# Kernel tuning notes

Hardware: AMD Instinct MI355X
Metric: run time of the kernel (lower is better)

The kernel has to match this reference:

```python
import jax, jax.numpy as jnp
import numpy as np
import math

EMBED_DIM = 1024
NUM_HEADS = 16
D_K = EMBED_DIM // NUM_HEADS
B, S = 2, 2048


def setup_inputs() -> dict:
    key = jax.random.key(0)
    ks = jax.random.split(key, 6)
    scale = 1.0 / math.sqrt(EMBED_DIM)
    x = jax.random.normal(ks[0], (B, S, EMBED_DIM), dtype=jnp.float32)
    mask = jax.random.randint(ks[1], (B, S), 0, 2) > 0  # True = masked-out key
    wq = jax.random.normal(ks[2], (EMBED_DIM, EMBED_DIM), dtype=jnp.float32) * scale
    wk = jax.random.normal(ks[3], (EMBED_DIM, EMBED_DIM), dtype=jnp.float32) * scale
    wv = jax.random.normal(ks[4], (EMBED_DIM, EMBED_DIM), dtype=jnp.float32) * scale
    wo = jax.random.normal(ks[5], (EMBED_DIM, EMBED_DIM), dtype=jnp.float32) * scale
    return {"x": x, "mask": mask, "wq": wq, "wk": wk, "wv": wv, "wo": wo}


def reference(x, mask, wq, wk, wv, wo):
    b, s, _ = x.shape
    # torch nn.Linear(bias=False): y = x @ W.T
    q = (x @ wq.T).reshape(b, s, NUM_HEADS, D_K).transpose(0, 2, 1, 3)  # [B,H,S,Dk]
    k = (x @ wk.T).reshape(b, s, NUM_HEADS, D_K).transpose(0, 2, 1, 3)
    v = (x @ wv.T).reshape(b, s, NUM_HEADS, D_K).transpose(0, 2, 1, 3)
    scores = jnp.einsum('bhqd,bhkd->bhqk', q, k) / math.sqrt(D_K)
    # mask [B,S] -> [B,1,1,S]: key-padding mask, True filled with -1e9
    scores = jnp.where(mask[:, None, None, :], jnp.float32(-1e9), scores)
    attn = jax.nn.softmax(scores, axis=-1)
    # dropout in eval mode -> identity
    out = jnp.einsum('bhqk,bhkd->bhqd', attn, v)
    out = out.transpose(0, 2, 1, 3).reshape(b, s, EMBED_DIM)
    return out @ wo.T
```

## Files before the change

kernel.cpp:

```cpp
#include <hip/hip_runtime.h>
#include <hip/hip_bf16.h>


typedef unsigned short u16;
typedef unsigned int u32;
using short8 = __attribute__((ext_vector_type(8))) short;
using f32x4  = __attribute__((ext_vector_type(4))) float;

#define WS_XB    0u
#define WS_WQKV  8388608u
#define WS_WOB   14680064u
#define WS_QB    16777216u
#define WS_KB    25165824u
#define WS_VTB   33554432u
#define WS_OB    41943040u

__device__ __forceinline__ u16 f2bf(float f) {
  u32 u = __float_as_uint(f);
  u += 0x7fffu + ((u >> 16) & 1u);
  return (u16)(u >> 16);
}

__device__ __forceinline__ ushort4 pk4(f32x4 v) {
  ushort4 r; r.x = f2bf(v[0]); r.y = f2bf(v[1]); r.z = f2bf(v[2]); r.w = f2bf(v[3]);
  return r;
}

__device__ __forceinline__ u32 pkbf2(float lo, float hi) {
  union { __hip_bfloat162 b; u32 u; } c;
  c.b = __float22bfloat162_rn(make_float2(lo, hi));
  return c.u;
}

__device__ __forceinline__ void gload16(const void* g, void* l) {
  __builtin_amdgcn_global_load_lds(
      (const __attribute__((address_space(1))) u32*)g,
      (__attribute__((address_space(3))) u32*)l, 16, 0, 0);
}

#define KSCALE 0.18033688011112042f

__global__ void convert_k(const float* __restrict__ x, const float* __restrict__ wq,
                          const float* __restrict__ wk, const float* __restrict__ wv,
                          const float* __restrict__ wo,
                          u16* __restrict__ xb, u16* __restrict__ wqkv, u16* __restrict__ wob) {
  size_t g = ((size_t)blockIdx.x * 256 + threadIdx.x) * 4;
  const float* s; u16* d;
  if (g < 4194304u)      { s = x  + g;            d = xb   + g; }
  else if (g < 5242880u) { s = wq + (g - 4194304u); d = wqkv + (g - 4194304u); }
  else if (g < 6291456u) { s = wk + (g - 5242880u); d = wqkv + 1048576u + (g - 5242880u); }
  else if (g < 7340032u) { s = wv + (g - 6291456u); d = wqkv + 2097152u + (g - 6291456u); }
  else                   { s = wo + (g - 7340032u); d = wob  + (g - 7340032u); }
  float4 v = *(const float4*)s;
  f32x4 vv = {v.x, v.y, v.z, v.w};
  *(ushort4*)d = pk4(vv);
}

__global__ void gemm_qkv(const u16* __restrict__ A, const u16* __restrict__ Bt,
                         u16* __restrict__ qb, u16* __restrict__ kb, u16* __restrict__ vtb) {
  __shared__ __align__(16) u16 As[128 * 64];
  __shared__ __align__(16) u16 Bs[128 * 64];
  const int tid  = threadIdx.x;
  const int wave = tid >> 6, lane = tid & 63;
  const int c16  = lane & 15, quad = lane >> 4;
  const int tile_m = blockIdx.x * 128;
  const int tile_n = blockIdx.y * 128;
  const int wm = (wave >> 1) * 64, wn = (wave & 1) * 64;
  const int srow = wave * 32 + (lane >> 3);
  const int sc   = lane & 7;
  const int which = blockIdx.y >> 3;
  const bool swp  = (which < 2);

  const u16* Pa = swp ? Bs : As;
  const u16* Pb = swp ? As : Bs;
  const int  ra = swp ? wn : wm;
  const int  rb = swp ? wm : wn;

  f32x4 acc[4][4] = {};

  for (int k0 = 0; k0 < 1024; k0 += 64) {
    __syncthreads();
#pragma unroll
    for (int j = 0; j < 4; ++j) {
      int row = srow + j * 8;
      int cp  = sc ^ (row & 7);
      gload16(A  + (size_t)(tile_m + row) * 1024 + k0 + cp * 8, As + row * 64 + sc * 8);
      gload16(Bt + (size_t)(tile_n + row) * 1024 + k0 + cp * 8, Bs + row * 64 + sc * 8);
    }
    __syncthreads();
#pragma unroll
    for (int kc = 0; kc < 2; ++kc) {
      const int ch = ((kc * 4 + quad) ^ (c16 & 7)) * 8;
      short8 fa[4], fb[4];
#pragma unroll
      for (int i = 0; i < 4; ++i)
        fa[i] = *(const short8*)(Pa + (ra + i * 16 + c16) * 64 + ch);
#pragma unroll
      for (int j = 0; j < 4; ++j)
        fb[j] = *(const short8*)(Pb + (rb + j * 16 + c16) * 64 + ch);
#pragma unroll
      for (int i = 0; i < 4; ++i)
#pragma unroll
        for (int j = 0; j < 4; ++j)
          acc[i][j] = __builtin_amdgcn_mfma_f32_16x16x32_bf16(fa[i], fb[j], acc[i][j], 0, 0, 0);
    }
  }

  if (which == 2) {
#pragma unroll
    for (int i = 0; i < 4; ++i) {
      int m0 = tile_m + wm + i * 16 + quad * 4;
      int bb = m0 >> 11, ss0 = m0 & 2047;
#pragma unroll
      for (int j = 0; j < 4; ++j) {
        int f = (tile_n & 1023) + wn + j * 16 + c16;
        int h = f >> 6, d = f & 63;
        *(ushort4*)(vtb + ((size_t)(bb * 16 + h) * 64 + d) * 2048 + ss0) = pk4(acc[i][j]);
      }
    }
  } else {
    u16* dstb = which ? kb : qb;
#pragma unroll
    for (int i = 0; i < 4; ++i) {
      int full = (tile_n & 1023) + wn + i * 16 + quad * 4;
      int h = full >> 6, d0 = full & 63;
#pragma unroll
      for (int j = 0; j < 4; ++j) {
        int t = tile_m + wm + j * 16 + c16;
        int bb = t >> 11, ss = t & 2047;
        f32x4 v = acc[i][j];
        if (which == 0) { v[0] *= KSCALE; v[1] *= KSCALE; v[2] *= KSCALE; v[3] *= KSCALE; }
        *(ushort4*)(dstb + ((size_t)(bb * 16 + h) * 2048 + ss) * 64 + d0) = pk4(v);
      }
    }
  }
}

__global__ __launch_bounds__(256) void attn_k(const u16* __restrict__ qb, const u16* __restrict__ kb,
                                              const u16* __restrict__ vtb, const int* __restrict__ mask,
                                              u16* __restrict__ ob) {
  __shared__ __align__(16) u16 Ks[2][64 * 64];
  __shared__ __align__(16) u16 Vs[2][64 * 64];
  __shared__ __align__(16) u16 Ps[128 * 64];
  __shared__ u32 mask2[1024];

  const int tid  = threadIdx.x;
  const int wave = tid >> 6, lane = tid & 63;
  const int c16  = lane & 15, g4 = lane >> 4;
  const int bh   = blockIdx.y;
  const int bidx = bh >> 4, h = bh & 15;
  const int q0   = blockIdx.x * 128;

  {
    int4 m0 = *(const int4*)(mask + bidx * 2048 + tid * 8);
    int4 m1 = *(const int4*)(mask + bidx * 2048 + tid * 8 + 4);
    uint4 dd;
    dd.x = (m0.x ? 0u : 0xFFFFu) | (m0.y ? 0u : 0xFFFF0000u);
    dd.y = (m0.z ? 0u : 0xFFFFu) | (m0.w ? 0u : 0xFFFF0000u);
    dd.z = (m1.x ? 0u : 0xFFFFu) | (m1.y ? 0u : 0xFFFF0000u);
    dd.w = (m1.z ? 0u : 0xFFFFu) | (m1.w ? 0u : 0xFFFF0000u);
    *(uint4*)(mask2 + tid * 4) = dd;
  }

  const u16* qg = qb + ((size_t)bh * 2048 + q0 + wave * 32) * 64;
  short8 qf[2][2];
#pragma unroll
  for (int kc = 0; kc < 2; ++kc)
#pragma unroll
    for (int nj = 0; nj < 2; ++nj)
      qf[kc][nj] = *(const short8*)(qg + (nj * 16 + c16) * 64 + kc * 32 + g4 * 8);

  const u16* kg = kb  + (size_t)bh * 2048 * 64;
  const u16* vg = vtb + (size_t)bh * 64 * 2048;
  {
#pragma unroll
    for (int j = 0; j < 2; ++j) {
      int r  = j * 32 + (tid >> 3);
      int cp = (tid & 7) ^ (r & 7);
      gload16(kg + (size_t)r * 64 + cp * 8,   &Ks[0][j * 2048 + tid * 8]);
      gload16(vg + (size_t)r * 2048 + cp * 8, &Vs[0][j * 2048 + tid * 8]);
    }
  }
  __syncthreads();

  short8 ones;
#pragma unroll
  for (int i = 0; i < 8; ++i) ones[i] = (short)0x3F80;

  f32x4 O[2][4] = {};
  f32x4 L[2] = {};

#pragma unroll 2
  for (int kt = 0; kt < 32; ++kt) {
    if (kt) __syncthreads();
    if (kt + 1 < 32) {
      const int nb = (kt + 1) & 1;
#pragma unroll
      for (int j = 0; j < 2; ++j) {
        int r  = j * 32 + (tid >> 3);
        int cp = (tid & 7) ^ (r & 7);
        gload16(kg + (size_t)((kt + 1) * 64 + r) * 64 + cp * 8, &Ks[nb][j * 2048 + tid * 8]);
        gload16(vg + (size_t)r * 2048 + (kt + 1) * 64 + cp * 8, &Vs[nb][j * 2048 + tid * 8]);
      }
    }
    const u16* ksb = Ks[kt & 1];
    const u16* vsb = Vs[kt & 1];

    f32x4 S[4][2] = {};
#pragma unroll
    for (int kc = 0; kc < 2; ++kc) {
      const int ch = ((kc * 4 + g4) ^ (c16 & 7)) * 8;
      short8 a[4];
#pragma unroll
      for (int mi = 0; mi < 4; ++mi)
        a[mi] = *(const short8*)(ksb + (mi * 16 + c16) * 64 + ch);
#pragma unroll
      for (int mi = 0; mi < 4; ++mi)
#pragma unroll
        for (int nj = 0; nj < 2; ++nj)
          S[mi][nj] = __builtin_amdgcn_mfma_f32_16x16x32_bf16(a[mi], qf[kc][nj], S[mi][nj], 0, 0, 0);
    }

    uint2 mk[4];
#pragma unroll
    for (int mi = 0; mi < 4; ++mi)
      mk[mi] = *(const uint2*)(mask2 + kt * 32 + mi * 8 + g4 * 2);

#pragma unroll
    for (int nj = 0; nj < 2; ++nj) {
      const int q = wave * 32 + nj * 16 + c16;
#pragma unroll
      for (int mi = 0; mi < 4; ++mi) {
        float p0 = __builtin_amdgcn_exp2f(S[mi][nj][0]);
        float p1 = __builtin_amdgcn_exp2f(S[mi][nj][1]);
        float p2 = __builtin_amdgcn_exp2f(S[mi][nj][2]);
        float p3 = __builtin_amdgcn_exp2f(S[mi][nj][3]);
        u32 lo = pkbf2(p0, p1) & mk[mi].x;
        u32 hi = pkbf2(p2, p3) & mk[mi].y;
        uint2 pkd; pkd.x = lo; pkd.y = hi;
        const int c = mi * 2 + (g4 >> 1);
        *(uint2*)(Ps + q * 64 + ((c ^ (c16 & 7)) * 8 + (g4 & 1) * 4)) = pkd;
      }
    }

#pragma unroll
    for (int kc = 0; kc < 2; ++kc) {
      const int ch = ((kc * 4 + g4) ^ (c16 & 7)) * 8;
      short8 a2[2], b2[4];
#pragma unroll
      for (int mi = 0; mi < 2; ++mi)
        a2[mi] = *(const short8*)(Ps + (wave * 32 + mi * 16 + c16) * 64 + ch);
#pragma unroll
      for (int nd = 0; nd < 4; ++nd)
        b2[nd] = *(const short8*)(vsb + (nd * 16 + c16) * 64 + ch);
#pragma unroll
      for (int mi = 0; mi < 2; ++mi) {
#pragma unroll
        for (int nd = 0; nd < 4; ++nd)
          O[mi][nd] = __builtin_amdgcn_mfma_f32_16x16x32_bf16(a2[mi], b2[nd], O[mi][nd], 0, 0, 0);
        L[mi] = __builtin_amdgcn_mfma_f32_16x16x32_bf16(a2[mi], ones, L[mi], 0, 0, 0);
      }
    }
  }

  u16* og = ob + ((size_t)(bidx * 2048 + q0 + wave * 32)) * 1024 + h * 64;
#pragma unroll
  for (int mi = 0; mi < 2; ++mi) {
    f32x4 linv;
#pragma unroll
    for (int r = 0; r < 4; ++r) linv[r] = 1.f / L[mi][r];
#pragma unroll
    for (int r = 0; r < 4; ++r) {
      int qrow = mi * 16 + g4 * 4 + r;
#pragma unroll
      for (int nd = 0; nd < 4; ++nd)
        og[(size_t)qrow * 1024 + nd * 16 + c16] = f2bf(O[mi][nd][r] * linv[r]);
    }
  }
}

__global__ __launch_bounds__(256) void gemm_out(const u16* __restrict__ A, const u16* __restrict__ Bt,
                         float* __restrict__ out) {
  __shared__ __align__(16) u16 As[128 * 64];
  __shared__ __align__(16) u16 Bs[64 * 64];
  const int tid  = threadIdx.x;
  const int wave = tid >> 6, lane = tid & 63;
  const int c16  = lane & 15, quad = lane >> 4;
  const int tile_m = blockIdx.x * 128;
  const int tile_n = blockIdx.y * 64;
  const int wm = wave * 32;
  const int sc   = lane & 7;

  f32x4 acc[4][2] = {};

  for (int k0 = 0; k0 < 1024; k0 += 64) {
    __syncthreads();
    {
      int rowa = tid >> 1;
      int sca  = (tid & 1) * 4 + (sc & 3);
    }
#pragma unroll
    for (int j = 0; j < 4; ++j) {
      int row = (tid >> 3) + j * 32;
      int cp  = sc ^ (row & 7);
      gload16(A + (size_t)(tile_m + row) * 1024 + k0 + cp * 8, As + row * 64 + sc * 8);
    }
#pragma unroll
    for (int j = 0; j < 2; ++j) {
      int row = (tid >> 3) + j * 32;
      int cp  = sc ^ (row & 7);
      gload16(Bt + (size_t)(tile_n + row) * 1024 + k0 + cp * 8, Bs + row * 64 + sc * 8);
    }
    __syncthreads();
#pragma unroll
    for (int kc = 0; kc < 2; ++kc) {
      const int ch = ((kc * 4 + quad) ^ (c16 & 7)) * 8;
      short8 fa[4], fb[2];
#pragma unroll
      for (int i = 0; i < 4; ++i)
        fa[i] = *(const short8*)(Bs + (i * 16 + c16) * 64 + ch);
#pragma unroll
      for (int j = 0; j < 2; ++j)
        fb[j] = *(const short8*)(As + (wm + j * 16 + c16) * 64 + ch);
#pragma unroll
      for (int i = 0; i < 4; ++i)
#pragma unroll
        for (int j = 0; j < 2; ++j)
          acc[i][j] = __builtin_amdgcn_mfma_f32_16x16x32_bf16(fa[i], fb[j], acc[i][j], 0, 0, 0);
    }
  }
#pragma unroll
  for (int i = 0; i < 4; ++i) {
    int f0 = tile_n + i * 16 + quad * 4;
#pragma unroll
    for (int j = 0; j < 2; ++j) {
      int t = tile_m + wm + j * 16 + c16;
      *(f32x4*)(out + (size_t)t * 1024 + f0) = acc[i][j];
    }
  }
}

extern "C" void kernel_launch(void* const* d_in, const int* in_sizes, int n_in,
                              void* d_out, int out_size, void* d_ws, size_t ws_size,
                              hipStream_t stream) {
  (void)in_sizes; (void)n_in; (void)out_size; (void)ws_size;
  const float* x    = (const float*)d_in[0];
  const int*   mask = (const int*)d_in[1];
  const float* wq   = (const float*)d_in[2];
  const float* wk   = (const float*)d_in[3];
  const float* wv   = (const float*)d_in[4];
  const float* wo   = (const float*)d_in[5];
  float* out = (float*)d_out;
  char*  ws  = (char*)d_ws;

  u16* xb   = (u16*)(ws + WS_XB);
  u16* wqkv = (u16*)(ws + WS_WQKV);
  u16* wob  = (u16*)(ws + WS_WOB);
  u16* qbuf = (u16*)(ws + WS_QB);
  u16* kbuf = (u16*)(ws + WS_KB);
  u16* vtb  = (u16*)(ws + WS_VTB);
  u16* obuf = (u16*)(ws + WS_OB);

  convert_k<<<8192, 256, 0, stream>>>(x, wq, wk, wv, wo, xb, wqkv, wob);
  gemm_qkv<<<dim3(32, 24), 256, 0, stream>>>(xb, wqkv, qbuf, kbuf, vtb);
  attn_k<<<dim3(16, 32), 256, 0, stream>>>(qbuf, kbuf, vtb, mask, obuf);
  gemm_out<<<dim3(32, 16), 256, 0, stream>>>(obuf, wob, out);
}
```

Measured before the change: 192.0 us.

## Split attention key tiles across paired waves with 512-thread blocks and reduce

The attention kernel moves to 512 threads, with each pair of waves sharing a 32-query group and splitting every 64-key tile into two halves. Partial O and L accumulators are combined through shared memory at the end. The block index is remapped to interleave heads across blocks, and s_setprio is raised around the MFMA sections. This halves the serial MFMA/exp work per wave and adds wave-level parallelism. The cost is an extra shared-memory reduction and larger blocks, which may lower the number of resident blocks.

```diff
diff --git a/kernel.cpp b/kernel.cpp
--- a/kernel.cpp
+++ b/kernel.cpp
@@ -136,50 +136,50 @@
   }
 }
 
-__global__ __launch_bounds__(256) void attn_k(const u16* __restrict__ qb, const u16* __restrict__ kb,
+__global__ __launch_bounds__(512) void attn_k(const u16* __restrict__ qb, const u16* __restrict__ kb,
                                               const u16* __restrict__ vtb, const int* __restrict__ mask,
                                               u16* __restrict__ ob) {
-  __shared__ __align__(16) u16 Ks[2][64 * 64];
-  __shared__ __align__(16) u16 Vs[2][64 * 64];
-  __shared__ __align__(16) u16 Ps[128 * 64];
-  __shared__ u32 mask2[1024];
+  __shared__ __align__(16) char smem[53248];
+  u16* const KsB   = (u16*)smem;
+  u16* const VsB   = (u16*)(smem + 16384);
+  u16* const Ps    = (u16*)(smem + 32768);
+  u32* const mask2 = (u32*)(smem + 49152);
 
   const int tid  = threadIdx.x;
   const int wave = tid >> 6, lane = tid & 63;
   const int c16  = lane & 15, g4 = lane >> 4;
-  const int bh   = blockIdx.y;
+  const int qg   = wave >> 1;
+  const int kh   = wave & 1;
+
+  const int f    = blockIdx.x + 16 * blockIdx.y;
+  const int i64  = f >> 3;
+  const int bh   = (f & 7) * 4 + (i64 >> 4);
+  const int q0   = (i64 & 15) * 128;
   const int bidx = bh >> 4, h = bh & 15;
-  const int q0   = blockIdx.x * 128;
 
   {
-    int4 m0 = *(const int4*)(mask + bidx * 2048 + tid * 8);
-    int4 m1 = *(const int4*)(mask + bidx * 2048 + tid * 8 + 4);
-    uint4 dd;
+    int4 m0 = *(const int4*)(mask + bidx * 2048 + tid * 4);
+    uint2 dd;
     dd.x = (m0.x ? 0u : 0xFFFFu) | (m0.y ? 0u : 0xFFFF0000u);
     dd.y = (m0.z ? 0u : 0xFFFFu) | (m0.w ? 0u : 0xFFFF0000u);
-    dd.z = (m1.x ? 0u : 0xFFFFu) | (m1.y ? 0u : 0xFFFF0000u);
-    dd.w = (m1.z ? 0u : 0xFFFFu) | (m1.w ? 0u : 0xFFFF0000u);
-    *(uint4*)(mask2 + tid * 4) = dd;
-  }
-
-  const u16* qg = qb + ((size_t)bh * 2048 + q0 + wave * 32) * 64;
+    *(uint2*)(mask2 + tid * 2) = dd;
+  }
+
+  const u16* qg_ = qb + ((size_t)bh * 2048 + q0 + qg * 32) * 64;
   short8 qf[2][2];
 #pragma unroll
   for (int kc = 0; kc < 2; ++kc)
 #pragma unroll
     for (int nj = 0; nj < 2; ++nj)
-      qf[kc][nj] = *(const short8*)(qg + (nj * 16 + c16) * 64 + kc * 32 + g4 * 8);
+      qf[kc][nj] = *(const short8*)(qg_ + (nj * 16 + c16) * 64 + kc * 32 + g4 * 8);
 
   const u16* kg = kb  + (size_t)bh * 2048 * 64;
   const u16* vg = vtb + (size_t)bh * 64 * 2048;
   {
-#pragma unroll
-    for (int j = 0; j < 2; ++j) {
-      int r  = j * 32 + (tid >> 3);
-      int cp = (tid & 7) ^ (r & 7);
-      gload16(kg + (size_t)r * 64 + cp * 8,   &Ks[0][j * 2048 + tid * 8]);
-      gload16(vg + (size_t)r * 2048 + cp * 8, &Vs[0][j * 2048 + tid * 8]);
-    }
+    int r  = tid >> 3;
+    int cp = (tid & 7) ^ (r & 7);
+    gload16(kg + (size_t)r * 64 + cp * 8,   KsB + tid * 8);
+    gload16(vg + (size_t)r * 2048 + cp * 8, VsB + tid * 8);
   }
   __syncthreads();
 
@@ -195,42 +195,41 @@
     if (kt) __syncthreads();
     if (kt + 1 < 32) {
       const int nb = (kt + 1) & 1;
-#pragma unroll
-      for (int j = 0; j < 2; ++j) {
-        int r  = j * 32 + (tid >> 3);
-        int cp = (tid & 7) ^ (r & 7);
-        gload16(kg + (size_t)((kt + 1) * 64 + r) * 64 + cp * 8, &Ks[nb][j * 2048 + tid * 8]);
-        gload16(vg + (size_t)r * 2048 + (kt + 1) * 64 + cp * 8, &Vs[nb][j * 2048 + tid * 8]);
-      }
-    }
-    const u16* ksb = Ks[kt & 1];
-    const u16* vsb = Vs[kt & 1];
-
-    f32x4 S[4][2] = {};
+      int r  = tid >> 3;
+      int cp = (tid & 7) ^ (r & 7);
+      gload16(kg + (size_t)((kt + 1) * 64 + r) * 64 + cp * 8, KsB + nb * 4096 + tid * 8);
+      gload16(vg + (size_t)r * 2048 + (kt + 1) * 64 + cp * 8, VsB + nb * 4096 + tid * 8);
+    }
+    const u16* ksb = KsB + (kt & 1) * 4096;
+    const u16* vsb = VsB + (kt & 1) * 4096;
+
+    f32x4 S[2][2] = {};
+    __builtin_amdgcn_s_setprio(1);
 #pragma unroll
     for (int kc = 0; kc < 2; ++kc) {
       const int ch = ((kc * 4 + g4) ^ (c16 & 7)) * 8;
-      short8 a[4];
-#pragma unroll
-      for (int mi = 0; mi < 4; ++mi)
-        a[mi] = *(const short8*)(ksb + (mi * 16 + c16) * 64 + ch);
-#pragma unroll
-      for (int mi = 0; mi < 4; ++mi)
+      short8 a[2];
+#pragma unroll
+      for (int mi = 0; mi < 2; ++mi)
+        a[mi] = *(const short8*)(ksb + (kh * 32 + mi * 16 + c16) * 64 + ch);
+#pragma unroll
+      for (int mi = 0; mi < 2; ++mi)
 #pragma unroll
         for (int nj = 0; nj < 2; ++nj)
           S[mi][nj] = __builtin_amdgcn_mfma_f32_16x16x32_bf16(a[mi], qf[kc][nj], S[mi][nj], 0, 0, 0);
     }
-
-    uint2 mk[4];
-#pragma unroll
-    for (int mi = 0; mi < 4; ++mi)
-      mk[mi] = *(const uint2*)(mask2 + kt * 32 + mi * 8 + g4 * 2);
+    __builtin_amdgcn_s_setprio(0);
+
+    uint2 mk[2];
+#pragma unroll
+    for (int mi = 0; mi < 2; ++mi)
+      mk[mi] = *(const uint2*)(mask2 + kt * 32 + kh * 16 + mi * 8 + g4 * 2);
 
 #pragma unroll
     for (int nj = 0; nj < 2; ++nj) {
-      const int q = wave * 32 + nj * 16 + c16;
-#pragma unroll
-      for (int mi = 0; mi < 4; ++mi) {
+      const int q = qg * 32 + nj * 16 + c16;
+#pragma unroll
+      for (int mi = 0; mi < 2; ++mi) {
         float p0 = __builtin_amdgcn_exp2f(S[mi][nj][0]);
         float p1 = __builtin_amdgcn_exp2f(S[mi][nj][1]);
         float p2 = __builtin_amdgcn_exp2f(S[mi][nj][2]);
@@ -238,21 +237,21 @@
         u32 lo = pkbf2(p0, p1) & mk[mi].x;
         u32 hi = pkbf2(p2, p3) & mk[mi].y;
         uint2 pkd; pkd.x = lo; pkd.y = hi;
-        const int c = mi * 2 + (g4 >> 1);
+        const int c = kh * 4 + mi * 2 + (g4 >> 1);
         *(uint2*)(Ps + q * 64 + ((c ^ (c16 & 7)) * 8 + (g4 & 1) * 4)) = pkd;
       }
     }
 
-#pragma unroll
-    for (int kc = 0; kc < 2; ++kc) {
-      const int ch = ((kc * 4 + g4) ^ (c16 & 7)) * 8;
+    {
+      const int ch = ((kh * 4 + g4) ^ (c16 & 7)) * 8;
       short8 a2[2], b2[4];
 #pragma unroll
       for (int mi = 0; mi < 2; ++mi)
-        a2[mi] = *(const short8*)(Ps + (wave * 32 + mi * 16 + c16) * 64 + ch);
+        a2[mi] = *(const short8*)(Ps + (qg * 32 + mi * 16 + c16) * 64 + ch);
 #pragma unroll
       for (int nd = 0; nd < 4; ++nd)
         b2[nd] = *(const short8*)(vsb + (nd * 16 + c16) * 64 + ch);
+      __builtin_amdgcn_s_setprio(1);
 #pragma unroll
       for (int mi = 0; mi < 2; ++mi) {
 #pragma unroll
@@ -260,22 +259,41 @@
           O[mi][nd] = __builtin_amdgcn_mfma_f32_16x16x32_bf16(a2[mi], b2[nd], O[mi][nd], 0, 0, 0);
         L[mi] = __builtin_amdgcn_mfma_f32_16x16x32_bf16(a2[mi], ones, L[mi], 0, 0, 0);
       }
-    }
-  }
-
-  u16* og = ob + ((size_t)(bidx * 2048 + q0 + wave * 32)) * 1024 + h * 64;
-#pragma unroll
-  for (int mi = 0; mi < 2; ++mi) {
-    f32x4 linv;
-#pragma unroll
-    for (int r = 0; r < 4; ++r) linv[r] = 1.f / L[mi][r];
-#pragma unroll
-    for (int r = 0; r < 4; ++r) {
-      int qrow = mi * 16 + g4 * 4 + r;
-#pragma unroll
-      for (int nd = 0; nd < 4; ++nd)
-        og[(size_t)qrow * 1024 + nd * 16 + c16] = f2bf(O[mi][nd][r] * linv[r]);
-    }
+      __builtin_amdgcn_s_setprio(0);
+    }
+  }
+
+  __syncthreads();
+  float* const redO = (float*)smem;
+  float* const redL = (float*)(smem + 33792);
+  if (kh) {
+#pragma unroll
+    for (int mi = 0; mi < 2; ++mi)
+#pragma unroll
+      for (int r = 0; r < 4; ++r) {
+        int row = qg * 32 + mi * 16 + g4 * 4 + r;
+#pragma unroll
+        for (int nd = 0; nd < 4; ++nd)
+          redO[row * 66 + nd * 16 + c16] = O[mi][nd][r];
+        if (c16 == 0) redL[row] = L[mi][r];
+      }
+  }
+  __syncthreads();
+  if (!kh) {
+    u16* og = ob + ((size_t)(bidx * 2048 + q0 + qg * 32)) * 1024 + h * 64;
+#pragma unroll
+    for (int mi = 0; mi < 2; ++mi)
+#pragma unroll
+      for (int r = 0; r < 4; ++r) {
+        int row  = qg * 32 + mi * 16 + g4 * 4 + r;
+        int qrow = mi * 16 + g4 * 4 + r;
+        float linv = 1.f / (L[mi][r] + redL[row]);
+#pragma unroll
+        for (int nd = 0; nd < 4; ++nd) {
+          float o = O[mi][nd][r] + redO[row * 66 + nd * 16 + c16];
+          og[(size_t)qrow * 1024 + nd * 16 + c16] = f2bf(o * linv);
+        }
+      }
   }
 }
 
@@ -295,10 +313,6 @@
 
   for (int k0 = 0; k0 < 1024; k0 += 64) {
     __syncthreads();
-    {
-      int rowa = tid >> 1;
-      int sca  = (tid & 1) * 4 + (sc & 3);
-    }
 #pragma unroll
     for (int j = 0; j < 4; ++j) {
       int row = (tid >> 3) + j * 32;
@@ -363,6 +377,6 @@
 
   convert_k<<<8192, 256, 0, stream>>>(x, wq, wk, wv, wo, xb, wqkv, wob);
   gemm_qkv<<<dim3(32, 24), 256, 0, stream>>>(xb, wqkv, qbuf, kbuf, vtb);
-  attn_k<<<dim3(16, 32), 256, 0, stream>>>(qbuf, kbuf, vtb, mask, obuf);
+  attn_k<<<dim3(16, 32), 512, 0, stream>>>(qbuf, kbuf, vtb, mask, obuf);
   gemm_out<<<dim3(32, 16), 256, 0, stream>>>(obuf, wob, out);
 }
```

Result: faster. 179.7 us (median of 2 runs) (-6.4%).
